# Optimization experiments

Hardware: AMD Instinct MI355X
Metric: run time of the kernel (lower is better)

Reference implementation:

```python
import jax, jax.numpy as jnp
import numpy as np

B, T, C, H = 4, 4096, 1024, 64

def setup_inputs() -> dict:
    key = jax.random.key(0)
    kx, kq, kk, kv = jax.random.split(key, 4)
    # nn.Linear weights are [out, in]; we store them that way and use einsum.
    s = 1.0 / np.sqrt(C)
    return {
        "x": jax.random.normal(kx, (B, T, C), dtype=jnp.float32),
        "Wq": jax.random.uniform(kq, (H, C), dtype=jnp.float32, minval=-s, maxval=s),
        "Wk": jax.random.uniform(kk, (H, C), dtype=jnp.float32, minval=-s, maxval=s),
        "Wv": jax.random.uniform(kv, (H, C), dtype=jnp.float32, minval=-s, maxval=s),
    }

def reference(x, Wq, Wk, Wv):
    # x: [B, T, C]; W*: [H, C] (torch Linear layout)
    Q = jnp.einsum('btc,hc->bth', x, Wq)  # [B, T, H]
    K = jnp.einsum('btc,hc->bth', x, Wk)
    V = jnp.einsum('btc,hc->bth', x, Wv)
    scale = K.shape[-1] ** -0.5
    scores = jnp.einsum('bqh,bkh->bqk', Q, K) * scale  # [B, T, T]
    Tn = x.shape[1]
    causal = jnp.tril(jnp.ones((Tn, Tn), dtype=bool))
    scores = jnp.where(causal, scores, -jnp.inf)
    attn = jax.nn.softmax(scores, axis=-1)
    return jnp.einsum('bqk,bkh->bqh', attn, V)  # [B, T, H]
```

## Files before the change

### kernel.cpp

```cpp
#include <hip/hip_runtime.h>
#include <hip/hip_bf16.h>

#define B_ 4
#define T_ 4096
#define C_ 1024
#define H_ 64

typedef __bf16 bf16x8 __attribute__((ext_vector_type(8)));
typedef float f32x4 __attribute__((ext_vector_type(4)));
typedef unsigned short u16x8 __attribute__((ext_vector_type(8)));

union Frag8 { uint4 u; bf16x8 b; u16x8 s; };

__device__ inline unsigned short bfbits(float f) {
  union { __hip_bfloat16 h; unsigned short u; } cv;
  cv.h = __float2bfloat16(f);
  return cv.u;
}

__device__ inline float b2f(unsigned u) {
  union { unsigned i; float f; } c; c.i = u << 16; return c.f;
}

__device__ inline bf16x8 ldb8(const unsigned short* p) {
  Frag8 f; f.u = *(const uint4*)p; return f.b;
}

__device__ inline bf16x8 asbf(uint4 u) { Frag8 f; f.u = u; return f.b; }

__device__ inline unsigned pkbf(float a, float b) {
  union { float f; unsigned u; } ua, ub; ua.f = a; ub.f = b;
  return __builtin_amdgcn_perm(ub.u + 0x8000u, ua.u + 0x8000u, 0x07060302u);
}

__device__ inline Frag8 packA(float4 a0, float4 a1) {
  Frag8 af;
  af.s[0] = bfbits(a0.x); af.s[1] = bfbits(a0.y);
  af.s[2] = bfbits(a0.z); af.s[3] = bfbits(a0.w);
  af.s[4] = bfbits(a1.x); af.s[5] = bfbits(a1.y);
  af.s[6] = bfbits(a1.z); af.s[7] = bfbits(a1.w);
  return af;
}

__device__ inline void gload16(const void* g, void* l) {
  __builtin_amdgcn_global_load_lds(
      (const __attribute__((address_space(1))) unsigned int*)g,
      (__attribute__((address_space(3))) unsigned int*)l, 16, 0, 0);
}

__global__ __launch_bounds__(256) void wconv(const float* __restrict__ Wq,
                                             const float* __restrict__ Wk,
                                             const float* __restrict__ Wv,
                                             unsigned short* __restrict__ Wb) {
  int i = blockIdx.x * 256 + threadIdx.x;
  size_t e = (size_t)i * 4;
  const float* src = (e < 65536) ? (Wq + e)
                   : (e < 131072 ? (Wk + (e - 65536)) : (Wv + (e - 131072)));
  float4 v = *(const float4*)src;
  unsigned long long o =
      (unsigned long long)bfbits(v.x)
    | ((unsigned long long)bfbits(v.y) << 16)
    | ((unsigned long long)bfbits(v.z) << 32)
    | ((unsigned long long)bfbits(v.w) << 48);
  *(unsigned long long*)(Wb + e) = o;
}

__global__ __launch_bounds__(256) void qkv_proj(const float* __restrict__ x,
                                                const unsigned short* __restrict__ Wb,
                                                unsigned short* __restrict__ qkv,
                                                unsigned short* __restrict__ Vt) {
  __shared__ float xs[2048];
  __shared__ unsigned short Wsh[12288];
  const int lane = threadIdx.x & 63;
  const int wave = threadIdx.x >> 6;
  const int q16 = lane & 15, quad = lane >> 4;
  const int x7 = q16 & 7;
  const size_t row0 = (size_t)blockIdx.x * 32;

  const int sr = lane >> 4;
  const int sc_pos = lane & 15;
  const int rloc = lane >> 3;
  const int cpos = lane & 7;

  f32x4 acc[2][3] = {};

  for (int kc = 0; kc < C_; kc += 64) {
    __syncthreads();
#pragma unroll
    for (int ii = 0; ii < 2; ++ii) {
      int i = wave * 2 + ii;
      int r = i * 4 + sr;
      int sg = (sc_pos >> 1) ^ (r & 7);
      const float* gp = x + (row0 + r) * C_ + kc + sg * 8 + (sc_pos & 1) * 4;
      gload16(gp, &xs[i * 256]);
    }
#pragma unroll
    for (int jj = 0; jj < 6; ++jj) {
      int j = wave * 6 + jj;
      int g = j * 8 + rloc;
      const unsigned short* gp = Wb + (size_t)(g >> 6) * 65536
                                    + (size_t)(g & 63) * C_ + kc + (cpos ^ rloc) * 8;
      gload16(gp, &Wsh[j * 512]);
    }
    __syncthreads();
#pragma unroll
    for (int s = 0; s < 2; ++s) {
      bf16x8 bf[3];
#pragma unroll
      for (int ct = 0; ct < 3; ++ct) {
        int g = wave * 48 + ct * 16 + q16;
        bf[ct] = ldb8(&Wsh[g * 64 + (((s * 4 + quad) ^ x7) * 8)]);
      }
#pragma unroll
      for (int rt = 0; rt < 2; ++rt) {
        int r = rt * 16 + q16;
        int p = ((s * 4 + quad) ^ (r & 7)) * 8;
        const float* ap = &xs[r * 64 + p];
        float4 a0 = *(const float4*)ap;
        float4 a1 = *(const float4*)(ap + 4);
        Frag8 af = packA(a0, a1);
#pragma unroll
        for (int ct = 0; ct < 3; ++ct)
          acc[rt][ct] = __builtin_amdgcn_mfma_f32_16x16x32_bf16(
              af.b, bf[ct], acc[rt][ct], 0, 0, 0);
      }
    }
  }

  const int bb = (int)(blockIdx.x >> 7);
#pragma unroll
  for (int rt = 0; rt < 2; ++rt) {
    const int t0 = (int)(row0 - (size_t)bb * T_) + rt * 16 + quad * 4;
#pragma unroll
    for (int ct = 0; ct < 3; ++ct) {
      int gcol = wave * 48 + ct * 16;
      int mat = gcol >> 6, h = (gcol & 63) + q16;
      if (mat == 2) {
        ushort4 v;
        v.x = bfbits(acc[rt][ct][0]); v.y = bfbits(acc[rt][ct][1]);
        v.z = bfbits(acc[rt][ct][2]); v.w = bfbits(acc[rt][ct][3]);
        *(ushort4*)(Vt + ((size_t)bb * H_ + h) * T_ + t0) = v;
      } else {
        float scale = (mat == 0) ? 0.18033688f : 1.0f;
#pragma unroll
        for (int r = 0; r < 4; ++r) {
          size_t row = row0 + rt * 16 + quad * 4 + r;
          qkv[(size_t)mat * 1048576 + row * H_ + h] = bfbits(acc[rt][ct][r] * scale);
        }
      }
    }
  }
}

__global__ __launch_bounds__(256) void attn(const unsigned short* __restrict__ Q,
                                            const unsigned short* __restrict__ K,
                                            const unsigned short* __restrict__ Vt,
                                            float* __restrict__ part) {
  const int b = blockIdx.x >> 6;
  const int qblk = 63 - (blockIdx.x & 63);
  const int ki = qblk + 1;
  const int c = blockIdx.y;
  const int c8 = c * 8;
  if (c8 >= ki) return;
  const int kend = (ki < c8 + 8) ? ki : c8 + 8;

  __shared__ unsigned short Ks[4096];
  __shared__ unsigned short Vs[4096];
  const int lane = threadIdx.x & 63;
  const int wave = threadIdx.x >> 6;
  const int q16 = lane & 15, quad = lane >> 4;
  const int x7 = q16 & 7;
  const int rloc = lane >> 3, cpos = lane & 7;

  const unsigned short* Qb = Q + (size_t)b * T_ * H_;
  const unsigned short* Kb = K + (size_t)b * T_ * H_;
  const unsigned short* Vtb = Vt + (size_t)b * H_ * T_;

  const int q0w = qblk * 64 + wave * 16;
  bf16x8 qf0 = ldb8(Qb + (size_t)(q0w + q16) * H_ + quad * 8);
  bf16x8 qf1 = ldb8(Qb + (size_t)(q0w + q16) * H_ + 32 + quad * 8);

  f32x4 o0 = {0.f, 0.f, 0.f, 0.f}, o1 = o0, o2 = o0, o3 = o0;
  float m = -3.0e38f, l = 0.0f;
  const int q_abs = q0w + q16;
  const int src0 = q16 + 32 * (quad & 1);
  const int kbsel = quad >> 1;

  for (int kt = c8; kt < kend; ++kt) {
    const int kkb = kt * 64;
    __syncthreads();
#pragma unroll
    for (int ii = 0; ii < 2; ++ii) {
      int i = wave * 2 + ii;
      gload16(Kb + (size_t)(kkb + i * 8 + rloc) * H_ + (cpos ^ rloc) * 8,
              &Ks[i * 512]);
      gload16(Vtb + (size_t)(i * 8 + rloc) * T_ + kkb + (cpos ^ rloc) * 8,
              &Vs[i * 512]);
    }
    __syncthreads();

    f32x4 st[4];
#pragma unroll
    for (int kb = 0; kb < 4; ++kb) {
      bf16x8 ka0 = ldb8(&Ks[(kb * 16 + q16) * 64 + ((quad ^ x7) * 8)]);
      bf16x8 ka1 = ldb8(&Ks[(kb * 16 + q16) * 64 + (((quad + 4) ^ x7) * 8)]);
      f32x4 s = {0.f, 0.f, 0.f, 0.f};
      s = __builtin_amdgcn_mfma_f32_16x16x32_bf16(ka0, qf0, s, 0, 0, 0);
      s = __builtin_amdgcn_mfma_f32_16x16x32_bf16(ka1, qf1, s, 0, 0, 0);
      st[kb] = s;
    }
    if (kt == ki - 1) {
#pragma unroll
      for (int kb = 0; kb < 4; ++kb)
#pragma unroll
        for (int r = 0; r < 4; ++r)
          if (kkb + kb * 16 + quad * 4 + r > q_abs) st[kb][r] = -3.0e38f;
    }

    float mloc = fmaxf(fmaxf(st[0][0], st[0][1]), fmaxf(st[0][2], st[0][3]));
#pragma unroll
    for (int kb = 1; kb < 4; ++kb)
      mloc = fmaxf(mloc, fmaxf(fmaxf(st[kb][0], st[kb][1]), fmaxf(st[kb][2], st[kb][3])));
    mloc = fmaxf(mloc, __shfl_xor(mloc, 16));
    mloc = fmaxf(mloc, __shfl_xor(mloc, 32));
    float mnew = fmaxf(m, mloc);
    float alpha = exp2f(m - mnew);
    float lsum = 0.f;
    unsigned pk[4][2];
#pragma unroll
    for (int kb = 0; kb < 4; ++kb) {
      float p0 = exp2f(st[kb][0] - mnew);
      float p1 = exp2f(st[kb][1] - mnew);
      float p2 = exp2f(st[kb][2] - mnew);
      float p3 = exp2f(st[kb][3] - mnew);
      lsum += (p0 + p1) + (p2 + p3);
      pk[kb][0] = pkbf(p0, p1);
      pk[kb][1] = pkbf(p2, p3);
    }
    lsum += __shfl_xor(lsum, 16);
    lsum += __shfl_xor(lsum, 32);
    l = l * alpha + lsum;
    m = mnew;
    float ar0 = __shfl(alpha, quad * 4 + 0);
    float ar1 = __shfl(alpha, quad * 4 + 1);
    float ar2 = __shfl(alpha, quad * 4 + 2);
    float ar3 = __shfl(alpha, quad * 4 + 3);
    o0[0] *= ar0; o0[1] *= ar1; o0[2] *= ar2; o0[3] *= ar3;
    o1[0] *= ar0; o1[1] *= ar1; o1[2] *= ar2; o1[3] *= ar3;
    o2[0] *= ar0; o2[1] *= ar1; o2[2] *= ar2; o2[3] *= ar3;
    o3[0] *= ar0; o3[1] *= ar1; o3[2] *= ar2; o3[3] *= ar3;

#pragma unroll
    for (int kb2 = 0; kb2 < 2; ++kb2) {
      int xA = __shfl((int)pk[2 * kb2][0], src0);
      int xB = __shfl((int)pk[2 * kb2 + 1][0], src0);
      int yA = __shfl((int)pk[2 * kb2][1], src0);
      int yB = __shfl((int)pk[2 * kb2 + 1][1], src0);
      int zA = __shfl((int)pk[2 * kb2][0], src0 + 16);
      int zB = __shfl((int)pk[2 * kb2 + 1][0], src0 + 16);
      int wA = __shfl((int)pk[2 * kb2][1], src0 + 16);
      int wB = __shfl((int)pk[2 * kb2 + 1][1], src0 + 16);
      Frag8 pf;
      pf.u.x = (unsigned)(kbsel ? xB : xA);
      pf.u.y = (unsigned)(kbsel ? yB : yA);
      pf.u.z = (unsigned)(kbsel ? zB : zA);
      pf.u.w = (unsigned)(kbsel ? wB : wA);
      int vp = ((kb2 * 4 + quad) ^ x7) * 8;
      bf16x8 v0 = ldb8(&Vs[(q16 + 0)  * 64 + vp]);
      bf16x8 v1 = ldb8(&Vs[(q16 + 16) * 64 + vp]);
      bf16x8 v2 = ldb8(&Vs[(q16 + 32) * 64 + vp]);
      bf16x8 v3 = ldb8(&Vs[(q16 + 48) * 64 + vp]);
      o0 = __builtin_amdgcn_mfma_f32_16x16x32_bf16(pf.b, v0, o0, 0, 0, 0);
      o1 = __builtin_amdgcn_mfma_f32_16x16x32_bf16(pf.b, v1, o1, 0, 0, 0);
      o2 = __builtin_amdgcn_mfma_f32_16x16x32_bf16(pf.b, v2, o2, 0, 0, 0);
      o3 = __builtin_amdgcn_mfma_f32_16x16x32_bf16(pf.b, v3, o3, 0, 0, 0);
    }
  }

  const int qtl = qblk * 4 + wave;
  float* Pf = part + ((size_t)((b << 8) + qtl) * 8 + c) * 544;
  unsigned* Pw = (unsigned*)Pf;
  Pw[0 * 64 + lane] = pkbf(o0[0], o0[1]);
  Pw[1 * 64 + lane] = pkbf(o0[2], o0[3]);
  Pw[2 * 64 + lane] = pkbf(o1[0], o1[1]);
  Pw[3 * 64 + lane] = pkbf(o1[2], o1[3]);
  Pw[4 * 64 + lane] = pkbf(o2[0], o2[1]);
  Pw[5 * 64 + lane] = pkbf(o2[2], o2[3]);
  Pw[6 * 64 + lane] = pkbf(o3[0], o3[1]);
  Pw[7 * 64 + lane] = pkbf(o3[2], o3[3]);
  if (quad == 0) { Pf[512 + q16] = m; Pf[528 + q16] = l; }
}

__global__ __launch_bounds__(256) void attn_merge(const float* __restrict__ part,
                                                  float* __restrict__ out) {
  const int qt = blockIdx.x;
  const int qtl = qt & 255, b = qt >> 8;
  const int ki = (qtl >> 2) + 1;
  const int nch = (ki + 7) >> 3;
  const int t = threadIdx.x;
  const int row = t >> 4, col0 = (t & 15) * 4;
  const int i = (col0 >> 4) * 4 + (row & 3);
  const int lane0 = (row >> 2) * 16 + (col0 & 15);
  const int sh = 16 * (i & 1);
  const float* P0 = part + (size_t)qt * 8 * 544;
  float M = -3.0e38f;
  for (int c2 = 0; c2 < nch; ++c2) M = fmaxf(M, P0[c2 * 544 + 512 + row]);
  float L = 0.f;
  float ax = 0.f, ay = 0.f, az = 0.f, aw = 0.f;
  for (int c2 = 0; c2 < nch; ++c2) {
    const float* P = P0 + c2 * 544;
    float w = exp2f(P[512 + row] - M);
    L += w * P[528 + row];
    const unsigned* Pw = (const unsigned*)P;
    uint4 wd = *(const uint4*)&Pw[(i >> 1) * 64 + lane0];
    ax += w * b2f((wd.x >> sh) & 0xffffu);
    ay += w * b2f((wd.y >> sh) & 0xffffu);
    az += w * b2f((wd.z >> sh) & 0xffffu);
    aw += w * b2f((wd.w >> sh) & 0xffffu);
  }
  float inv = 1.0f / L;
  float4 r = {ax * inv, ay * inv, az * inv, aw * inv};
  *(float4*)(out + ((size_t)b * T_ + qtl * 16 + row) * H_ + col0) = r;
}

extern "C" void kernel_launch(void* const* d_in, const int* in_sizes, int n_in,
                              void* d_out, int out_size, void* d_ws, size_t ws_size,
                              hipStream_t stream) {
  const float* x  = (const float*)d_in[0];
  const float* Wq = (const float*)d_in[1];
  const float* Wk = (const float*)d_in[2];
  const float* Wv = (const float*)d_in[3];
  float* out = (float*)d_out;
  unsigned short* ws = (unsigned short*)d_ws;

  unsigned short* Wb  = ws;
  unsigned short* qkv = ws + 196608;
  unsigned short* Vt  = qkv + (size_t)2 * 1048576;
  float* part = (float*)(ws + 196608 + (size_t)3 * 1048576);

  wconv<<<192, 256, 0, stream>>>(Wq, Wk, Wv, Wb);
  qkv_proj<<<512, 256, 0, stream>>>(x, Wb, qkv, Vt);
  attn<<<dim3(256, 8), 256, 0, stream>>>(qkv, qkv + 1048576, Vt, part);
  attn_merge<<<1024, 256, 0, stream>>>(part, out);
}
```

Before: 170.2 us.

## Double-buffer LDS tiles in QKV projection and attention kernels

Both the QKV projection and the attention kernel now keep two shared-memory buffers and issue the global-to-LDS loads for the next tile before computing on the current one. This cuts one barrier per iteration and lets memory loads overlap with MFMA work. The cost is doubled LDS use (about 56KB in qkv_proj), which may lower occupancy. Correctness depends on gload16's wait semantics, since the async loads must have landed before the end-of-iteration barrier.

```diff
diff --git a/kernel.cpp b/kernel.cpp
--- a/kernel.cpp
+++ b/kernel.cpp
@@ -69,8 +69,8 @@
                                                 const unsigned short* __restrict__ Wb,
                                                 unsigned short* __restrict__ qkv,
                                                 unsigned short* __restrict__ Vt) {
-  __shared__ float xs[2048];
-  __shared__ unsigned short Wsh[12288];
+  __shared__ float xs[2][2048];
+  __shared__ unsigned short Wsh[2][12288];
   const int lane = threadIdx.x & 63;
   const int wave = threadIdx.x >> 6;
   const int q16 = lane & 15, quad = lane >> 4;
@@ -84,15 +84,14 @@
 
   f32x4 acc[2][3] = {};
 
-  for (int kc = 0; kc < C_; kc += 64) {
-    __syncthreads();
+  auto stage = [&](int buf, int kc) {
 #pragma unroll
     for (int ii = 0; ii < 2; ++ii) {
       int i = wave * 2 + ii;
       int r = i * 4 + sr;
       int sg = (sc_pos >> 1) ^ (r & 7);
       const float* gp = x + (row0 + r) * C_ + kc + sg * 8 + (sc_pos & 1) * 4;
-      gload16(gp, &xs[i * 256]);
+      gload16(gp, &xs[buf][i * 256]);
     }
 #pragma unroll
     for (int jj = 0; jj < 6; ++jj) {
@@ -100,22 +99,31 @@
       int g = j * 8 + rloc;
       const unsigned short* gp = Wb + (size_t)(g >> 6) * 65536
                                     + (size_t)(g & 63) * C_ + kc + (cpos ^ rloc) * 8;
-      gload16(gp, &Wsh[j * 512]);
-    }
-    __syncthreads();
+      gload16(gp, &Wsh[buf][j * 512]);
+    }
+  };
+
+  stage(0, 0);
+  __syncthreads();
+
+  int cur = 0;
+  for (int t = 0; t < 16; ++t) {
+    if (t < 15) stage(cur ^ 1, (t + 1) * 64);
+    const float* Xc = xs[cur];
+    const unsigned short* Wc = Wsh[cur];
 #pragma unroll
     for (int s = 0; s < 2; ++s) {
       bf16x8 bf[3];
 #pragma unroll
       for (int ct = 0; ct < 3; ++ct) {
         int g = wave * 48 + ct * 16 + q16;
-        bf[ct] = ldb8(&Wsh[g * 64 + (((s * 4 + quad) ^ x7) * 8)]);
+        bf[ct] = ldb8(&Wc[g * 64 + (((s * 4 + quad) ^ x7) * 8)]);
       }
 #pragma unroll
       for (int rt = 0; rt < 2; ++rt) {
         int r = rt * 16 + q16;
         int p = ((s * 4 + quad) ^ (r & 7)) * 8;
-        const float* ap = &xs[r * 64 + p];
+        const float* ap = &Xc[r * 64 + p];
         float4 a0 = *(const float4*)ap;
         float4 a1 = *(const float4*)(ap + 4);
         Frag8 af = packA(a0, a1);
@@ -125,6 +133,8 @@
               af.b, bf[ct], acc[rt][ct], 0, 0, 0);
       }
     }
+    __syncthreads();
+    cur ^= 1;
   }
 
   const int bb = (int)(blockIdx.x >> 7);
@@ -164,8 +174,8 @@
   if (c8 >= ki) return;
   const int kend = (ki < c8 + 8) ? ki : c8 + 8;
 
-  __shared__ unsigned short Ks[4096];
-  __shared__ unsigned short Vs[4096];
+  __shared__ unsigned short Ks[2][4096];
+  __shared__ unsigned short Vs[2][4096];
   const int lane = threadIdx.x & 63;
   const int wave = threadIdx.x >> 6;
   const int q16 = lane & 15, quad = lane >> 4;
@@ -176,6 +186,18 @@
   const unsigned short* Kb = K + (size_t)b * T_ * H_;
   const unsigned short* Vtb = Vt + (size_t)b * H_ * T_;
 
+  auto stage = [&](int buf, int kt) {
+    const int kkb = kt * 64;
+#pragma unroll
+    for (int ii = 0; ii < 2; ++ii) {
+      int i = wave * 2 + ii;
+      gload16(Kb + (size_t)(kkb + i * 8 + rloc) * H_ + (cpos ^ rloc) * 8,
+              &Ks[buf][i * 512]);
+      gload16(Vtb + (size_t)(i * 8 + rloc) * T_ + kkb + (cpos ^ rloc) * 8,
+              &Vs[buf][i * 512]);
+    }
+  };
+
   const int q0w = qblk * 64 + wave * 16;
   bf16x8 qf0 = ldb8(Qb + (size_t)(q0w + q16) * H_ + quad * 8);
   bf16x8 qf1 = ldb8(Qb + (size_t)(q0w + q16) * H_ + 32 + quad * 8);
@@ -186,24 +208,21 @@
   const int src0 = q16 + 32 * (quad & 1);
   const int kbsel = quad >> 1;
 
+  stage(0, c8);
+  __syncthreads();
+
+  int cur = 0;
   for (int kt = c8; kt < kend; ++kt) {
     const int kkb = kt * 64;
-    __syncthreads();
-#pragma unroll
-    for (int ii = 0; ii < 2; ++ii) {
-      int i = wave * 2 + ii;
-      gload16(Kb + (size_t)(kkb + i * 8 + rloc) * H_ + (cpos ^ rloc) * 8,
-              &Ks[i * 512]);
-      gload16(Vtb + (size_t)(i * 8 + rloc) * T_ + kkb + (cpos ^ rloc) * 8,
-              &Vs[i * 512]);
-    }
-    __syncthreads();
+    if (kt + 1 < kend) stage(cur ^ 1, kt + 1);
+    const unsigned short* Kc = Ks[cur];
+    const unsigned short* Vc = Vs[cur];
 
     f32x4 st[4];
 #pragma unroll
     for (int kb = 0; kb < 4; ++kb) {
-      bf16x8 ka0 = ldb8(&Ks[(kb * 16 + q16) * 64 + ((quad ^ x7) * 8)]);
-      bf16x8 ka1 = ldb8(&Ks[(kb * 16 + q16) * 64 + (((quad + 4) ^ x7) * 8)]);
+      bf16x8 ka0 = ldb8(&Kc[(kb * 16 + q16) * 64 + ((quad ^ x7) * 8)]);
+      bf16x8 ka1 = ldb8(&Kc[(kb * 16 + q16) * 64 + (((quad + 4) ^ x7) * 8)]);
       f32x4 s = {0.f, 0.f, 0.f, 0.f};
       s = __builtin_amdgcn_mfma_f32_16x16x32_bf16(ka0, qf0, s, 0, 0, 0);
       s = __builtin_amdgcn_mfma_f32_16x16x32_bf16(ka1, qf1, s, 0, 0, 0);
@@ -266,15 +285,17 @@
       pf.u.z = (unsigned)(kbsel ? zB : zA);
       pf.u.w = (unsigned)(kbsel ? wB : wA);
       int vp = ((kb2 * 4 + quad) ^ x7) * 8;
-      bf16x8 v0 = ldb8(&Vs[(q16 + 0)  * 64 + vp]);
-      bf16x8 v1 = ldb8(&Vs[(q16 + 16) * 64 + vp]);
-      bf16x8 v2 = ldb8(&Vs[(q16 + 32) * 64 + vp]);
-      bf16x8 v3 = ldb8(&Vs[(q16 + 48) * 64 + vp]);
+      bf16x8 v0 = ldb8(&Vc[(q16 + 0)  * 64 + vp]);
+      bf16x8 v1 = ldb8(&Vc[(q16 + 16) * 64 + vp]);
+      bf16x8 v2 = ldb8(&Vc[(q16 + 32) * 64 + vp]);
+      bf16x8 v3 = ldb8(&Vc[(q16 + 48) * 64 + vp]);
       o0 = __builtin_amdgcn_mfma_f32_16x16x32_bf16(pf.b, v0, o0, 0, 0, 0);
       o1 = __builtin_amdgcn_mfma_f32_16x16x32_bf16(pf.b, v1, o1, 0, 0, 0);
       o2 = __builtin_amdgcn_mfma_f32_16x16x32_bf16(pf.b, v2, o2, 0, 0, 0);
       o3 = __builtin_amdgcn_mfma_f32_16x16x32_bf16(pf.b, v3, o3, 0, 0, 0);
     }
+    __syncthreads();
+    cur ^= 1;
   }
 
   const int qtl = qblk * 4 + wave;
```

New measurement: 161.6 us. 5.1% less time.
